# Performance work log

Measured on AMD Instinct MI355X. Metric: run time of the kernel, lower is better.

The kernel has to match this reference:

```python
import jax, jax.numpy as jnp
import numpy as np

N_NODES = 1000
HIDDEN = 256
IN_DIM = 128
N_EDGES = 64000


def setup_inputs() -> dict:
    key = jax.random.key(0)
    ks = jax.random.split(key, 24)
    inp = {
        "x": jax.random.normal(ks[0], (N_NODES, IN_DIM), dtype=jnp.float32),
        "edge_index": jax.random.randint(ks[1], (2, N_EDGES), 0, N_NODES, dtype=jnp.int64),
    }
    dims = [(HIDDEN, 2 * IN_DIM)] + [(HIDDEN, 2 * HIDDEN)] * 4
    for l, (dout, din) in enumerate(dims):
        s0 = 1.0 / np.sqrt(din)
        s1 = 1.0 / np.sqrt(HIDDEN)
        inp[f"w{l}_0"] = jax.random.normal(ks[2 + 4 * l], (dout, din), dtype=jnp.float32) * s0
        inp[f"b{l}_0"] = jax.random.normal(ks[3 + 4 * l], (dout,), dtype=jnp.float32) * s0
        inp[f"w{l}_1"] = jax.random.normal(ks[4 + 4 * l], (HIDDEN, HIDDEN), dtype=jnp.float32) * s1
        inp[f"b{l}_1"] = jax.random.normal(ks[5 + 4 * l], (HIDDEN,), dtype=jnp.float32) * s1
    return inp


def _edge_conv(x, src, dst, w1, b1, w2, b2):
    # gather endpoint features per edge: [E, D]
    x_i = x[dst]  # destination (edge_index[1])
    x_j = x[src]  # source (edge_index[0])
    m = jnp.concatenate([x_i, x_j - x_i], axis=-1)  # [E, 2D]
    h = jax.nn.relu(m @ w1.T + b1) @ w2.T + b2      # 2-layer MLP, [E, HIDDEN]
    # scatter-max to destination nodes (include_self=False -> empty rows = 0)
    agg = jax.ops.segment_max(h, dst, num_segments=N_NODES)
    agg = jnp.where(jnp.isneginf(agg), jnp.zeros((), agg.dtype), agg)
    return jax.nn.relu(agg)


def reference(x, edge_index, w0_0, b0_0, w0_1, b0_1, w1_0, b1_0, w1_1, b1_1,
              w2_0, b2_0, w2_1, b2_1, w3_0, b3_0, w3_1, b3_1, w4_0, b4_0, w4_1, b4_1):
    src = edge_index[0]
    dst = edge_index[1]
    params = [(w0_0, b0_0, w0_1, b0_1), (w1_0, b1_0, w1_1, b1_1),
              (w2_0, b2_0, w2_1, b2_1), (w3_0, b3_0, w3_1, b3_1),
              (w4_0, b4_0, w4_1, b4_1)]
    h = x
    for (w1, b1, w2, b2) in params:
        h = _edge_conv(h, src, dst, w1, b1, w2, b2)
    return h
```

## Files before the change

### kernel.cpp

```cpp
#include <hip/hip_runtime.h>

#define NN 1000
#define NE 64000
#define HH 256

typedef _Float16 half8 __attribute__((ext_vector_type(8)));
typedef float floatx4 __attribute__((ext_vector_type(4)));

struct PrepArgs { const float* w0[5]; const float* w1[5]; };


template <int NK>
__device__ __forceinline__ void node_tile(const float* __restrict__ X,
                                          const _Float16* __restrict__ Wn,
                                          const float* __restrict__ b0,
                                          _Float16* __restrict__ out, int bid) {
    const int Kd = NK * 32;
    int t = threadIdx.x;
    int wave = t >> 6, lane = t & 63;
    int q = lane >> 4, mn = lane & 15;
    int m0 = (bid % 63) * 16;
    int n0 = (bid / 63) * 128 + wave * 32;
    int slice = (bid / 63) * 4 + wave;
    int rr = m0 + mn;
    if (rr >= NN) rr = NN - 1;

    half8 afa[NK];
    half8 bfa[NK][2];
#pragma unroll
    for (int kk = 0; kk < NK; kk++) {
        int ka = kk * 32 + q * 8;
        const float* p = X + (size_t)rr * Kd + ka;
        floatx4 x0 = *(const floatx4*)p;
        floatx4 x1 = *(const floatx4*)(p + 4);
        half8 aa;
#pragma unroll
        for (int j = 0; j < 4; j++) { aa[j] = (_Float16)x0[j]; aa[4 + j] = (_Float16)x1[j]; }
        afa[kk] = aa;
        bfa[kk][0] = *(const half8*)(Wn + (((slice * NK + kk) * 2 + 0) * 64 + lane) * 8);
        bfa[kk][1] = *(const half8*)(Wn + (((slice * NK + kk) * 2 + 1) * 64 + lane) * 8);
    }
    floatx4 acc[2] = {};
#pragma unroll
    for (int kk = 0; kk < NK; kk++) {
        acc[0] = __builtin_amdgcn_mfma_f32_16x16x32_f16(afa[kk], bfa[kk][0], acc[0], 0, 0, 0);
        acc[1] = __builtin_amdgcn_mfma_f32_16x16x32_f16(afa[kk], bfa[kk][1], acc[1], 0, 0, 0);
    }
#pragma unroll
    for (int nt = 0; nt < 2; nt++) {
        int col = n0 + nt * 16 + mn;
        float bias = (col < 256) ? b0[col] : 0.f;
#pragma unroll
        for (int r2 = 0; r2 < 4; r2++) {
            int orow = m0 + q * 4 + r2;
            if (orow < NN)
                out[(size_t)orow * 512 + col] = (_Float16)(acc[nt][r2] + bias);
        }
    }
}

__device__ __forceinline__ void node_tile0(const float* __restrict__ X,
                                           const float* __restrict__ w0,
                                           const float* __restrict__ b0,
                                           _Float16* __restrict__ out, int bid) {
    const int NK = 4;
    const int Kd = 128;
    int t = threadIdx.x;
    int wave = t >> 6, lane = t & 63;
    int q = lane >> 4, mn = lane & 15;
    int m0 = (bid % 63) * 16;
    int n0 = (bid / 63) * 128 + wave * 32;
    int slice = (bid / 63) * 4 + wave;
    int rr = m0 + mn;
    if (rr >= NN) rr = NN - 1;

    half8 afa[NK];
    half8 bfa[NK][2];
#pragma unroll
    for (int kk = 0; kk < NK; kk++) {
        int ka = kk * 32 + q * 8;
        const float* p = X + (size_t)rr * Kd + ka;
        floatx4 x0 = *(const floatx4*)p;
        floatx4 x1 = *(const floatx4*)(p + 4);
        half8 aa;
#pragma unroll
        for (int j = 0; j < 4; j++) { aa[j] = (_Float16)x0[j]; aa[4 + j] = (_Float16)x1[j]; }
        afa[kk] = aa;
#pragma unroll
        for (int nt = 0; nt < 2; nt++) {
            int n = slice * 32 + nt * 16 + mn;
            int k = kk * 32 + q * 8;
            half8 bb;
            if (n < 256) {
                const float* pa = w0 + (size_t)n * 256 + k;
                floatx4 a0 = *(const floatx4*)pa;
                floatx4 a1 = *(const floatx4*)(pa + 4);
                floatx4 c0 = *(const floatx4*)(pa + 128);
                floatx4 c1 = *(const floatx4*)(pa + 132);
#pragma unroll
                for (int j = 0; j < 4; j++) {
                    bb[j] = (_Float16)(a0[j] - c0[j]);
                    bb[4 + j] = (_Float16)(a1[j] - c1[j]);
                }
            } else {
                const float* pb = w0 + (size_t)(n - 256) * 256 + 128 + k;
                floatx4 c0 = *(const floatx4*)pb;
                floatx4 c1 = *(const floatx4*)(pb + 4);
#pragma unroll
                for (int j = 0; j < 4; j++) {
                    bb[j] = (_Float16)c0[j];
                    bb[4 + j] = (_Float16)c1[j];
                }
            }
            bfa[kk][nt] = bb;
        }
    }
    floatx4 acc[2] = {};
#pragma unroll
    for (int kk = 0; kk < NK; kk++) {
        acc[0] = __builtin_amdgcn_mfma_f32_16x16x32_f16(afa[kk], bfa[kk][0], acc[0], 0, 0, 0);
        acc[1] = __builtin_amdgcn_mfma_f32_16x16x32_f16(afa[kk], bfa[kk][1], acc[1], 0, 0, 0);
    }
#pragma unroll
    for (int nt = 0; nt < 2; nt++) {
        int col = n0 + nt * 16 + mn;
        float bias = (col < 256) ? b0[col] : 0.f;
#pragma unroll
        for (int r2 = 0; r2 < 4; r2++) {
            int orow = m0 + q * 4 + r2;
            if (orow < NN)
                out[(size_t)orow * 512 + col] = (_Float16)(acc[nt][r2] + bias);
        }
    }
}

__global__ __launch_bounds__(256) void k_pre1(PrepArgs pa,
                                              const int* __restrict__ ei,
                                              const float* __restrict__ X,
                                              const float* __restrict__ b0_0,
                                              _Float16* __restrict__ node_ab,
                                              _Float16* wnode, _Float16* w2h,
                                              int* cnts16, int* cursor,
                                              float* agg0, float* dout) {
    int bid = blockIdx.x;
    int t = threadIdx.x;
    if (bid < 16) {
        int* my = cnts16 + bid * 1024;
        for (int i = t; i < 1024; i += 256) my[i] = 0;
        __syncthreads();
        for (int e = bid * 256 + t; e < NE; e += 16 * 256)
            atomicAdd(&my[ei[NE + e] & 1023], 1);
    } else if (bid < 16 + 252) {
        node_tile0(X, pa.w0[0], b0_0, node_ab, bid - 16);
    } else {
        int gtid = (bid - 268) * 256 + t;
        int gs = 256 * 256;
        for (int i = gtid; i < 1024; i += gs) cursor[i] = 0;
        for (int l = 1; l < 5; l++) {
            const float* w0 = pa.w0[l];
            _Float16* wn = wnode + l * 131072;
            for (int i = gtid; i < 131072; i += gs) {
                int j = i & 7;
                int lane = (i >> 3) & 63;
                int nt = (i >> 9) & 1;
                int kk = (i >> 10) & 7;
                int slice = i >> 13;
                int mn = lane & 15, q = lane >> 4;
                int n = slice * 32 + nt * 16 + mn;
                int k = kk * 32 + q * 8 + j;
                float v = (n < 256) ? (w0[n * 512 + k] - w0[n * 512 + 256 + k])
                                    : w0[(n - 256) * 512 + 256 + k];
                wn[i] = (_Float16)v;
            }
        }
        for (int l = 0; l < 5; l++) {
            const float* w1 = pa.w1[l];
            _Float16* w2 = w2h + l * 65536;
            for (int i = gtid; i < 65536; i += gs) {
                int j = i & 7;
                int lane = (i >> 3) & 63;
                int nt = (i >> 9) & 3;
                int kk = (i >> 11) & 7;
                int ws = (i >> 14) & 3;
                int mn = lane & 15, q = lane >> 4;
                int row = ws * 64 + nt * 16 + mn;
                int col = kk * 32 + q * 8 + j;
                w2[i] = (_Float16)w1[row * 256 + col];
            }
        }
        floatx4 z = {0.f, 0.f, 0.f, 0.f};
        floatx4* p4 = (floatx4*)agg0;
        for (int i = gtid; i < 4 * NN * HH / 4; i += gs) p4[i] = z;
        floatx4* o4 = (floatx4*)dout;
        for (int i = gtid; i < NN * HH / 4; i += gs) o4[i] = z;
    }
}

__global__ __launch_bounds__(256) void k_scatter2(const int* __restrict__ ei,
                                                  const int* __restrict__ cnts16,
                                                  int* __restrict__ cursor,
                                                  int* __restrict__ ssrc,
                                                  int4* __restrict__ table) {
    __shared__ int sbase[1024];
    __shared__ int ssum[256];
    __shared__ int schk[256];
    int t = threadIdx.x;
    int base = t * 4;
    int c4[4]; int sum = 0;
#pragma unroll
    for (int j = 0; j < 4; j++) {
        int c = 0;
#pragma unroll
        for (int b = 0; b < 16; b++) c += cnts16[b * 1024 + base + j];
        c4[j] = c; sum += c;
    }
    ssum[t] = sum;
    int ch4[4]; int csum = 0;
#pragma unroll
    for (int j = 0; j < 4; j++) { ch4[j] = (c4[j] + 63) >> 6; csum += ch4[j]; }
    schk[t] = csum;
    __syncthreads();
    for (int d = 1; d < 256; d <<= 1) {
        int v1 = (t >= d) ? ssum[t - d] : 0;
        int v2 = (t >= d) ? schk[t - d] : 0;
        __syncthreads();
        ssum[t] += v1;
        schk[t] += v2;
        __syncthreads();
    }
    int run = (t > 0) ? ssum[t - 1] : 0;
#pragma unroll
    for (int j = 0; j < 4; j++) { sbase[base + j] = run; run += c4[j]; }
    __syncthreads();
    if (blockIdx.x == 0) {
        int crun = (t > 0) ? schk[t - 1] : 0;
#pragma unroll
        for (int j = 0; j < 4; j++) {
            int d = base + j, c = c4[j], st = sbase[base + j], nc = ch4[j];
            for (int k = 0; k < nc; k++) {
                int len = c - k * 64; if (len > 64) len = 64;
                table[crun + k] = make_int4(d, st + k * 64, len, nc == 1 ? 1 : 0);
            }
            crun += nc;
        }
        int nch = schk[255];
        for (int i = nch + t; i < 2048; i += 256) table[i] = make_int4(0, 0, 0, 0);
    }
    for (int e = blockIdx.x * 256 + t; e < NE; e += gridDim.x * 256) {
        int s = ei[e] & 1023, d = ei[NE + e] & 1023;
        int pos = sbase[d] + atomicAdd(&cursor[d], 1);
        if (pos < NE) ssrc[pos] = s;
    }
}

__global__ __launch_bounds__(256) void k_node(const float* __restrict__ agg_in,
                                              const _Float16* __restrict__ Wn,
                                              const float* __restrict__ b0,
                                              _Float16* __restrict__ out) {
    node_tile<8>(agg_in, Wn, b0, out, blockIdx.x);
}

__global__ __launch_bounds__(1024, 4) void edge_gemm4(const _Float16* __restrict__ node_ab,
                          const int* __restrict__ ssrc,
                          const int4* __restrict__ table,
                          const _Float16* __restrict__ W2,
                          const float* __restrict__ b2,
                          float* __restrict__ agg) {
    __shared__ _Float16 h1[64 * 256];
    int t = threadIdx.x;
    int wave = t >> 6, lane = t & 63;
    int q = lane >> 4, mn = lane & 15;
    int s = lane & 31;
    int rp = t >> 5;

    const _Float16* Wb = W2 + (wave >> 2) * 16384 + (wave & 3) * 512 + (size_t)lane * 8;
    half8 w2r[8];
#pragma unroll
    for (int kk = 0; kk < 8; kk++)
        w2r[kk] = *(const half8*)(Wb + kk * 2048);
    float bias = b2[wave * 16 + mn];

    for (int i = 0; i < 8; i++) {
        int4 ck = table[blockIdx.x + i * 256];
        int len = ck.z;
        if (len == 0) continue;
        int dst = ck.x, start = ck.y, sole = ck.w;

        __syncthreads();
        {
            half8 av = *(const half8*)(node_ab + (size_t)dst * 512 + s * 8);
#pragma unroll
            for (int rr = 0; rr < 2; rr++) {
                int row = rp * 2 + rr;
                half8 hv = {};
                if (row < len) {
                    int sn = ssrc[start + row];
                    half8 bv = *(const half8*)(node_ab + (size_t)sn * 512 + 256 + s * 8);
                    hv = av + bv;
#pragma unroll
                    for (int j = 0; j < 8; j++) hv[j] = hv[j] > (_Float16)0 ? hv[j] : (_Float16)0;
                }
                int p = (s & ~7) | ((s ^ row) & 7);
                *(half8*)(&h1[row * 256 + p * 8]) = hv;
            }
        }
        __syncthreads();

        floatx4 acc[4] = {};
#pragma unroll
        for (int kk = 0; kk < 8; kk++) {
#pragma unroll
            for (int mt = 0; mt < 4; mt++) {
                int r = mt * 16 + mn;
                int c = kk * 4 + q;
                int p = (c & ~7) | ((c ^ r) & 7);
                half8 af = *(const half8*)(&h1[r * 256 + p * 8]);
                acc[mt] = __builtin_amdgcn_mfma_f32_16x16x32_f16(af, w2r[kk], acc[mt], 0, 0, 0);
            }
        }

        float m = -3.0e38f;
#pragma unroll
        for (int mt = 0; mt < 4; mt++) {
#pragma unroll
            for (int r2 = 0; r2 < 4; r2++) {
                int row = mt * 16 + q * 4 + r2;
                if (row < len) m = fmaxf(m, acc[mt][r2]);
            }
        }
        m = fmaxf(m, __shfl_xor(m, 16, 64));
        m = fmaxf(m, __shfl_xor(m, 32, 64));
        if (q == 0) {
            float v = m + bias;
            v = v > 0.f ? v : 0.f;
            float* p = agg + (size_t)dst * HH + wave * 16 + mn;
            if (sole) {
                *p = v;
            } else if (v > 0.f) {
                atomicMax((unsigned int*)p, __float_as_uint(v));
            }
        }
    }
}

extern "C" void kernel_launch(void* const* d_in, const int* in_sizes, int n_in,
                              void* d_out, int out_size, void* d_ws, size_t ws_size,
                              hipStream_t stream) {
    const float* x = (const float*)d_in[0];
    const int* ei = (const int*)d_in[1];
    PrepArgs pa;
    const float* b0s[5];
    const float* b1s[5];
    for (int l = 0; l < 5; l++) {
        pa.w0[l] = (const float*)d_in[2 + 4 * l];
        b0s[l] = (const float*)d_in[3 + 4 * l];
        pa.w1[l] = (const float*)d_in[4 + 4 * l];
        b1s[l] = (const float*)d_in[5 + 4 * l];
    }

    int* ssrc = (int*)d_ws;
    int* cnts16 = ssrc + NE;
    int* cursor = cnts16 + 16 * 1024;
    int4* table = (int4*)(cursor + 1024);
    _Float16* node_ab = (_Float16*)(table + 2048);
    float* agg0 = (float*)(node_ab + 1024 * 512);
    float* agg1 = agg0 + NN * HH;
    float* agg2 = agg1 + NN * HH;
    float* agg3 = agg2 + NN * HH;
    _Float16* wnode = (_Float16*)(agg3 + NN * HH);
    _Float16* w2h = wnode + 5 * 131072;

    hipLaunchKernelGGL(k_pre1, dim3(524), dim3(256), 0, stream,
                       pa, ei, x, b0s[0], node_ab, wnode, w2h,
                       cnts16, cursor, agg0, (float*)d_out);
    hipLaunchKernelGGL(k_scatter2, dim3(NE / 256), dim3(256), 0, stream,
                       ei, cnts16, cursor, ssrc, table);

    float* aggs[5] = {agg0, agg1, agg2, agg3, (float*)d_out};
    for (int l = 0; l < 5; l++) {
        hipLaunchKernelGGL(edge_gemm4, dim3(256), dim3(1024), 0, stream,
                           node_ab, ssrc, table, w2h + (size_t)l * 65536, b1s[l], aggs[l]);
        if (l < 4)
            hipLaunchKernelGGL(k_node, dim3(252), dim3(256), 0, stream,
                               aggs[l], wnode + (size_t)(l + 1) * 131072, b0s[l + 1], node_ab);
    }
}
```

Baseline: 263.2 us.

## Launch one 512-thread block per edge chunk instead of looping eight chunks

The edge GEMM kernel now launches 2048 blocks of 512 threads, one per table chunk, instead of 256 blocks of 1024 threads that each loop over eight chunks. Each wave now computes two 16-column output tiles and loads W2 fragments per k-step from global memory rather than keeping them in registers across chunks. This is meant to remove the per-chunk barriers and the serial chunk loop, and to let empty chunks exit early, so occupancy and latency hiding improve. In exchange, W2 is reloaded once per block, from L2 or global memory, instead of being reused across eight chunks.

```diff
diff --git a/kernel.cpp b/kernel.cpp
--- a/kernel.cpp
+++ b/kernel.cpp
@@ -260,80 +260,83 @@
     node_tile<8>(agg_in, Wn, b0, out, blockIdx.x);
 }
 
-__global__ __launch_bounds__(1024, 4) void edge_gemm4(const _Float16* __restrict__ node_ab,
+__global__ __launch_bounds__(512, 8) void edge_gemm5(const _Float16* __restrict__ node_ab,
                           const int* __restrict__ ssrc,
                           const int4* __restrict__ table,
                           const _Float16* __restrict__ W2,
                           const float* __restrict__ b2,
                           float* __restrict__ agg) {
     __shared__ _Float16 h1[64 * 256];
+    int4 ck = table[blockIdx.x];
+    int len = ck.z;
+    if (len == 0) return;
+    int dst = ck.x, start = ck.y, sole = ck.w;
     int t = threadIdx.x;
     int wave = t >> 6, lane = t & 63;
     int q = lane >> 4, mn = lane & 15;
-    int s = lane & 31;
-    int rp = t >> 5;
-
-    const _Float16* Wb = W2 + (wave >> 2) * 16384 + (wave & 3) * 512 + (size_t)lane * 8;
-    half8 w2r[8];
-#pragma unroll
-    for (int kk = 0; kk < 8; kk++)
-        w2r[kk] = *(const half8*)(Wb + kk * 2048);
-    float bias = b2[wave * 16 + mn];
-
-    for (int i = 0; i < 8; i++) {
-        int4 ck = table[blockIdx.x + i * 256];
-        int len = ck.z;
-        if (len == 0) continue;
-        int dst = ck.x, start = ck.y, sole = ck.w;
-
-        __syncthreads();
-        {
-            half8 av = *(const half8*)(node_ab + (size_t)dst * 512 + s * 8);
-#pragma unroll
-            for (int rr = 0; rr < 2; rr++) {
-                int row = rp * 2 + rr;
-                half8 hv = {};
-                if (row < len) {
-                    int sn = ssrc[start + row];
-                    half8 bv = *(const half8*)(node_ab + (size_t)sn * 512 + 256 + s * 8);
-                    hv = av + bv;
-#pragma unroll
-                    for (int j = 0; j < 8; j++) hv[j] = hv[j] > (_Float16)0 ? hv[j] : (_Float16)0;
-                }
-                int p = (s & ~7) | ((s ^ row) & 7);
-                *(half8*)(&h1[row * 256 + p * 8]) = hv;
-            }
-        }
-        __syncthreads();
-
-        floatx4 acc[4] = {};
-#pragma unroll
-        for (int kk = 0; kk < 8; kk++) {
-#pragma unroll
-            for (int mt = 0; mt < 4; mt++) {
-                int r = mt * 16 + mn;
-                int c = kk * 4 + q;
-                int p = (c & ~7) | ((c ^ r) & 7);
-                half8 af = *(const half8*)(&h1[r * 256 + p * 8]);
-                acc[mt] = __builtin_amdgcn_mfma_f32_16x16x32_f16(af, w2r[kk], acc[mt], 0, 0, 0);
-            }
-        }
-
-        float m = -3.0e38f;
+    const _Float16* W2w = W2 + (wave >> 1) * 16384 + ((wave & 1) * 2) * 512;
+
+    {
+        int s = t & 31;
+        int rg = t >> 5;
+        half8 av = *(const half8*)(node_ab + (size_t)dst * 512 + s * 8);
+#pragma unroll
+        for (int it = 0; it < 4; it++) {
+            int row = it * 16 + rg;
+            half8 hv = {};
+            if (row < len) {
+                int sn = ssrc[start + row];
+                half8 bv = *(const half8*)(node_ab + (size_t)sn * 512 + 256 + s * 8);
+                hv = av + bv;
+#pragma unroll
+                for (int j = 0; j < 8; j++) hv[j] = hv[j] > (_Float16)0 ? hv[j] : (_Float16)0;
+            }
+            int p = (s & ~7) | ((s ^ row) & 7);
+            *(half8*)(&h1[row * 256 + p * 8]) = hv;
+        }
+    }
+    __syncthreads();
+
+    floatx4 acc[4][2] = {};
+#pragma unroll
+    for (int kk = 0; kk < 8; kk++) {
+        half8 bf0 = *(const half8*)(W2w + kk * 2048 + (size_t)lane * 8);
+        half8 bf1 = *(const half8*)(W2w + kk * 2048 + 512 + (size_t)lane * 8);
 #pragma unroll
         for (int mt = 0; mt < 4; mt++) {
-#pragma unroll
-            for (int r2 = 0; r2 < 4; r2++) {
-                int row = mt * 16 + q * 4 + r2;
-                if (row < len) m = fmaxf(m, acc[mt][r2]);
-            }
-        }
-        m = fmaxf(m, __shfl_xor(m, 16, 64));
-        m = fmaxf(m, __shfl_xor(m, 32, 64));
-        if (q == 0) {
-            float v = m + bias;
+            int r = mt * 16 + mn;
+            int c = kk * 4 + q;
+            int p = (c & ~7) | ((c ^ r) & 7);
+            half8 af = *(const half8*)(&h1[r * 256 + p * 8]);
+            acc[mt][0] = __builtin_amdgcn_mfma_f32_16x16x32_f16(af, bf0, acc[mt][0], 0, 0, 0);
+            acc[mt][1] = __builtin_amdgcn_mfma_f32_16x16x32_f16(af, bf1, acc[mt][1], 0, 0, 0);
+        }
+    }
+
+    float m[2] = {-3.0e38f, -3.0e38f};
+#pragma unroll
+    for (int mt = 0; mt < 4; mt++) {
+#pragma unroll
+        for (int r2 = 0; r2 < 4; r2++) {
+            int row = mt * 16 + q * 4 + r2;
+            if (row < len) {
+                m[0] = fmaxf(m[0], acc[mt][0][r2]);
+                m[1] = fmaxf(m[1], acc[mt][1][r2]);
+            }
+        }
+    }
+#pragma unroll
+    for (int nt = 0; nt < 2; nt++) {
+        m[nt] = fmaxf(m[nt], __shfl_xor(m[nt], 16, 64));
+        m[nt] = fmaxf(m[nt], __shfl_xor(m[nt], 32, 64));
+    }
+    if (q == 0) {
+#pragma unroll
+        for (int nt = 0; nt < 2; nt++) {
+            int col = wave * 32 + nt * 16 + mn;
+            float v = m[nt] + b2[col];
             v = v > 0.f ? v : 0.f;
-            float* p = agg + (size_t)dst * HH + wave * 16 + mn;
+            float* p = agg + (size_t)dst * HH + col;
             if (sole) {
                 *p = v;
             } else if (v > 0.f) {
@@ -378,7 +381,7 @@
 
     float* aggs[5] = {agg0, agg1, agg2, agg3, (float*)d_out};
     for (int l = 0; l < 5; l++) {
-        hipLaunchKernelGGL(edge_gemm4, dim3(256), dim3(1024), 0, stream,
+        hipLaunchKernelGGL(edge_gemm5, dim3(2048), dim3(512), 0, stream,
                            node_ab, ssrc, table, w2h + (size_t)l * 65536, b1s[l], aggs[l]);
         if (l < 4)
             hipLaunchKernelGGL(k_node, dim3(252), dim3(256), 0, stream,
```

After: 240.1 us. -8.8%, faster.
